# Kernel optimization log

Measured on AMD Instinct MI355X. Metric: run time of the kernel, lower is better.

Reference implementation:

```python
import jax, jax.numpy as jnp
import numpy as np

D_MODEL = 1024
D_FF = 4096
NUM_HEADS = 16
D_HEAD = D_MODEL // NUM_HEADS
EPS = 1e-5


def setup_inputs() -> dict:
    key = jax.random.key(0)
    ks = jax.random.split(key, 16)
    s = 0.02
    return {
        "X": jax.random.normal(ks[0], (2, 2048, D_MODEL), dtype=jnp.float32),
        "W_qkv": jax.random.normal(ks[1], (D_MODEL, 3 * D_MODEL), dtype=jnp.float32) * s,
        "b_qkv": jax.random.normal(ks[2], (3 * D_MODEL,), dtype=jnp.float32) * s,
        "W_o": jax.random.normal(ks[3], (D_MODEL, D_MODEL), dtype=jnp.float32) * s,
        "b_o": jax.random.normal(ks[4], (D_MODEL,), dtype=jnp.float32) * s,
        "W_1": jax.random.normal(ks[5], (D_MODEL, D_FF), dtype=jnp.float32) * s,
        "b_1": jax.random.normal(ks[6], (D_FF,), dtype=jnp.float32) * s,
        "W_2": jax.random.normal(ks[7], (D_FF, D_MODEL), dtype=jnp.float32) * s,
        "b_2": jax.random.normal(ks[8], (D_MODEL,), dtype=jnp.float32) * s,
        "ln1_g": jnp.ones((D_MODEL,), dtype=jnp.float32),
        "ln1_b": jnp.zeros((D_MODEL,), dtype=jnp.float32),
        "ln2_g": jnp.ones((D_MODEL,), dtype=jnp.float32),
        "ln2_b": jnp.zeros((D_MODEL,), dtype=jnp.float32),
    }


def _layernorm(x, g, b):
    mu = jnp.mean(x, axis=-1, keepdims=True)
    var = jnp.mean(jnp.square(x - mu), axis=-1, keepdims=True)
    return (x - mu) * jax.lax.rsqrt(var + EPS) * g + b


def reference(X, W_qkv, b_qkv, W_o, b_o, W_1, b_1, W_2, b_2, ln1_g, ln1_b, ln2_g, ln2_b):
    B, T, D = X.shape
    qkv = X @ W_qkv + b_qkv                      # [B,T,3D]
    Q, K, V = jnp.split(qkv, 3, axis=-1)
    # [B,H,T,d]
    Q = Q.reshape(B, T, NUM_HEADS, D_HEAD).transpose(0, 2, 1, 3)
    K = K.reshape(B, T, NUM_HEADS, D_HEAD).transpose(0, 2, 1, 3)
    V = V.reshape(B, T, NUM_HEADS, D_HEAD).transpose(0, 2, 1, 3)
    scores = jnp.einsum('bhqd,bhkd->bhqk', Q, K) / np.float32(D_HEAD) ** 0.5
    causal = jnp.tril(jnp.ones((T, T), dtype=bool))
    scores = jnp.where(causal, scores, jnp.float32(-jnp.inf))
    A = jax.nn.softmax(scores, axis=-1)
    O = jnp.einsum('bhqk,bhkd->bhqd', A, V)
    O = O.transpose(0, 2, 1, 3).reshape(B, T, D)
    O = O @ W_o + b_o
    H_1 = _layernorm(X + O, ln1_g, ln1_b)
    H_2 = (jax.nn.gelu(H_1 @ W_1 + b_1, approximate=False)) @ W_2 + b_2
    return _layernorm(H_1 + H_2, ln2_g, ln2_b)
```

## Files before the change

### kernel.cpp

```cpp
#include <hip/hip_runtime.h>
#include <cmath>

typedef unsigned short u16;
typedef __bf16 bf16x8 __attribute__((ext_vector_type(8)));
typedef float f32x4 __attribute__((ext_vector_type(4)));

#define DEVI __device__ __forceinline__

DEVI float b2f(u16 u){ union{unsigned int i; float f;} v; v.i=(unsigned int)u<<16; return v.f; }
DEVI u16 f2b(float f){ union{unsigned int i; float f;} v; v.f=f;
    unsigned int r=(v.i+0x7FFFu+((v.i>>16)&1u))>>16; return (u16)r; }

DEVI void gload_lds16(const u16* g, u16* l){
    __builtin_amdgcn_global_load_lds((__attribute__((address_space(1))) void*)g,
                                     (__attribute__((address_space(3))) void*)l,
                                     16, 0, 0);
}

__global__ __launch_bounds__(256)
void cvt_bf16(const float* __restrict__ in, u16* __restrict__ out)
{
    const int i = (blockIdx.x * 256 + threadIdx.x) * 4;
    float4 v = *(const float4*)&in[i];
    ushort4 o;
    o.x = f2b(v.x); o.y = f2b(v.y); o.z = f2b(v.z); o.w = f2b(v.w);
    *(ushort4*)&out[i] = o;
}

__global__ __launch_bounds__(256)
void cvt_transpose(const float* __restrict__ in, u16* __restrict__ out, int R, int C)
{
    __shared__ __align__(16) u16 tile[64*72];
    const int rb = blockIdx.x*64, cb = blockIdx.y*64;
    const int t = threadIdx.x;
    const int r = t >> 3, c0 = (t & 7) * 8;
    #pragma unroll
    for (int rr = 0; rr < 2; rr++) {
        const int row = r + rr*32;
        float4 a = *(const float4*)&in[(long)(rb + row)*C + cb + c0];
        float4 b = *(const float4*)&in[(long)(rb + row)*C + cb + c0 + 4];
        u16* tp = &tile[row*72 + c0];
        tp[0]=f2b(a.x); tp[1]=f2b(a.y); tp[2]=f2b(a.z); tp[3]=f2b(a.w);
        tp[4]=f2b(b.x); tp[5]=f2b(b.y); tp[6]=f2b(b.z); tp[7]=f2b(b.w);
    }
    __syncthreads();
    #pragma unroll
    for (int rr = 0; rr < 2; rr++) {
        const int cr = r + rr*32;
        u16 tmp[8];
        #pragma unroll
        for (int j = 0; j < 8; j++) tmp[j] = tile[(c0 + j)*72 + cr];
        *(uint4*)&out[(long)(cb + cr)*R + rb + c0] = *(uint4*)tmp;
    }
}

template<int EPI, int BM>
__global__ __launch_bounds__(256)
void gemm_bt(const u16* __restrict__ A, const u16* __restrict__ Bt,
             const float* __restrict__ bias, const u16* __restrict__ Res,
             u16* __restrict__ C, int M, int N, int K)
{
    constexpr int RM = BM / 32;
    constexpr int NA = (BM / 16) * 2 / 4;
    __shared__ __align__(16) u16 As[BM*64];
    __shared__ __align__(16) u16 Bs[128*64];
    const int tid  = threadIdx.x;
    const int wave = tid >> 6, lane = tid & 63;
    const int tm = blockIdx.x * BM, tn = blockIdx.y * 128;

    const int rs = lane >> 2, cs = (lane & 3) * 8;
    const u16* gA[NA]; u16* lA[NA];
    #pragma unroll
    for (int i = 0; i < NA; i++) {
        const int c = wave + i*4;
        const int p = c / (BM/16), rb = c % (BM/16);
        gA[i] = A + (long)(tm + rb*16 + rs)*K + p*32 + cs;
        lA[i] = As + p*(BM*32) + rb*512;
    }
    const u16* gB[4]; u16* lB[4];
    #pragma unroll
    for (int i = 0; i < 4; i++) {
        const int c = wave + i*4;
        const int p = c >> 3, rb = c & 7;
        gB[i] = Bt + (long)(tn + rb*16 + rs)*K + p*32 + cs;
        lB[i] = Bs + p*(128*32) + rb*512;
    }

    const int wm = (wave >> 1) * (BM/2), wn = (wave & 1) * 64;
    const int fr = lane & 15, fq = lane >> 4;

    f32x4 acc[RM][4] = {};
    for (int k0 = 0; k0 < K; k0 += 64) {
        __syncthreads();
        #pragma unroll
        for (int i = 0; i < NA; i++) gload_lds16(gA[i] + k0, lA[i]);
        #pragma unroll
        for (int i = 0; i < 4; i++)  gload_lds16(gB[i] + k0, lB[i]);
        __syncthreads();
        #pragma unroll
        for (int p = 0; p < 2; p++) {
            bf16x8 af[RM], bfr[4];
            #pragma unroll
            for (int i = 0; i < RM; i++)
                af[i]  = *(const bf16x8*)&As[p*(BM*32) + (wm + i*16 + fr)*32 + fq*8];
            #pragma unroll
            for (int j = 0; j < 4; j++)
                bfr[j] = *(const bf16x8*)&Bs[p*(128*32) + (wn + j*16 + fr)*32 + fq*8];
            #pragma unroll
            for (int i = 0; i < RM; i++)
                #pragma unroll
                for (int j = 0; j < 4; j++)
                    acc[i][j] = __builtin_amdgcn_mfma_f32_16x16x32_bf16(af[i], bfr[j], acc[i][j], 0, 0, 0);
        }
    }

    #pragma unroll
    for (int i = 0; i < RM; i++) {
        const int row = tm + wm + i*16 + fq*4;
        #pragma unroll
        for (int j = 0; j < 4; j++) {
            const int col = tn + wn + j*16 + fr;
            const float bv = bias[col];
            #pragma unroll
            for (int r = 0; r < 4; r++) {
                float v = acc[i][j][r] + bv;
                const long idx = (long)(row + r)*N + col;
                if (EPI == 1) v += b2f(Res[idx]);
                if (EPI == 2) {
                    const float u = v + 0.044715f*v*v*v;
                    const float t = exp2f(u * 2.302208f);
                    v = v * t * __builtin_amdgcn_rcpf(t + 1.f);
                }
                C[idx] = f2b(v);
            }
        }
    }
}

__global__ __launch_bounds__(256)
void attn_kernel(const u16* __restrict__ qkv, u16* __restrict__ O)
{
    constexpr float LOG2E = 1.4426950408889634f;
    __shared__ __align__(16) u16 Qs[64*72];
    __shared__ __align__(16) u16 Ks[64*72];
    __shared__ __align__(16) u16 Vs[64*72];
    __shared__ __align__(16) u16 Ps[4][16*72];

    const int tid = threadIdx.x, wave = tid >> 6, lane = tid & 63;
    const int qt = blockIdx.x, h = blockIdx.y, b = blockIdx.z;
    const long base = (long)b*2048*3072 + h*64;
    const int fr = lane & 15, fq = lane >> 4;

    {
        const int r = tid >> 3, c = (tid & 7) * 8;
        #pragma unroll
        for (int rr = 0; rr < 2; rr++) {
            uint4 v = *(const uint4*)&qkv[base + (long)(qt*64 + r + rr*32)*3072 + c];
            u16 tmp[8]; *(uint4*)tmp = v;
            u16* qp = &Qs[(r + rr*32)*72 + c];
            #pragma unroll
            for (int j = 0; j < 8; j++) qp[j] = f2b(b2f(tmp[j]) * 0.125f);
        }
    }
    __syncthreads();

    bf16x8 bq[2];
    #pragma unroll
    for (int ks = 0; ks < 2; ks++)
        bq[ks] = *(const bf16x8*)&Qs[(wave*16 + fr)*72 + ks*32 + fq*8];

    const int q_glob = qt*64 + wave*16 + fr;
    f32x4 o[4] = {};
    float m_i = -1e30f, l_i = 0.f;

    for (int kt = 0; kt <= qt; kt++) {
        __syncthreads();
        {
            const int r = tid >> 3, c = (tid & 7) * 8;
            #pragma unroll
            for (int rr = 0; rr < 2; rr++) {
                const int row = r + rr*32;
                uint4 kv = *(const uint4*)&qkv[base + 1024 + (long)(kt*64 + row)*3072 + c];
                *(uint4*)&Ks[row*72 + c] = kv;
                uint4 vv = *(const uint4*)&qkv[base + 2048 + (long)(kt*64 + row)*3072 + c];
                u16 tmp[8]; *(uint4*)tmp = vv;
                #pragma unroll
                for (int j = 0; j < 8; j++) {
                    const int d = c + j;
                    Vs[d*72 + (row ^ (d & 56))] = tmp[j];
                }
            }
        }
        __syncthreads();

        f32x4 st[4] = {};
        #pragma unroll
        for (int nt = 0; nt < 4; nt++)
            #pragma unroll
            for (int ks = 0; ks < 2; ks++) {
                bf16x8 ak = *(const bf16x8*)&Ks[(nt*16 + fr)*72 + ks*32 + fq*8];
                st[nt] = __builtin_amdgcn_mfma_f32_16x16x32_bf16(ak, bq[ks], st[nt], 0, 0, 0);
            }

        float sv[4][4];
        float mx = -1e30f;
        #pragma unroll
        for (int nt = 0; nt < 4; nt++) {
            #pragma unroll
            for (int r = 0; r < 4; r++) {
                const int key = kt*64 + nt*16 + fq*4 + r;
                float v = st[nt][r];
                if (key > q_glob) v = -1e30f;
                sv[nt][r] = v;
                mx = fmaxf(mx, v);
            }
        }
        mx = fmaxf(mx, __shfl_xor(mx, 16, 64));
        mx = fmaxf(mx, __shfl_xor(mx, 32, 64));
        const float mnew  = fmaxf(m_i, mx);
        const float alpha = exp2f((m_i - mnew) * LOG2E);
        float ps = 0.f;
        #pragma unroll
        for (int nt = 0; nt < 4; nt++)
            #pragma unroll
            for (int r = 0; r < 4; r++) {
                const float p = exp2f((sv[nt][r] - mnew) * LOG2E);
                sv[nt][r] = p; ps += p;
            }
        ps += __shfl_xor(ps, 16, 64);
        ps += __shfl_xor(ps, 32, 64);
        l_i = l_i * alpha + ps;
        m_i = mnew;

        #pragma unroll
        for (int r = 0; r < 4; r++) {
            const float ar = __shfl(alpha, (lane & 48) + fq*4 + r, 64);
            #pragma unroll
            for (int dt = 0; dt < 4; dt++) o[dt][r] *= ar;
        }

        u16* pw = Ps[wave];
        #pragma unroll
        for (int nt = 0; nt < 4; nt++)
            #pragma unroll
            for (int d = 0; d < 2; d++) {
                const unsigned pk = (unsigned)f2b(sv[nt][2*d]) |
                                    ((unsigned)f2b(sv[nt][2*d+1]) << 16);
                *(unsigned*)&pw[fr*72 + nt*16 + fq*4 + 2*d] = pk;
            }
        __asm__ volatile("" ::: "memory");

        bf16x8 ap[2];
        #pragma unroll
        for (int kk = 0; kk < 2; kk++)
            ap[kk] = *(const bf16x8*)&pw[fr*72 + kk*32 + fq*8];

        #pragma unroll
        for (int dt = 0; dt < 4; dt++) {
            const int d = dt*16 + fr;
            #pragma unroll
            for (int kk = 0; kk < 2; kk++) {
                const int kb = (kk*32 + fq*8) ^ (d & 56);
                bf16x8 bv = *(const bf16x8*)&Vs[d*72 + kb];
                o[dt] = __builtin_amdgcn_mfma_f32_16x16x32_bf16(ap[kk], bv, o[dt], 0, 0, 0);
            }
        }
    }

    float lro[4];
    #pragma unroll
    for (int r = 0; r < 4; r++)
        lro[r] = __shfl(l_i, (lane & 48) + fq*4 + r, 64);
    const long orow0 = (long)b*2048 + qt*64 + wave*16 + fq*4;
    #pragma unroll
    for (int dt = 0; dt < 4; dt++) {
        const int col = h*64 + dt*16 + fr;
        #pragma unroll
        for (int r = 0; r < 4; r++)
            O[(orow0 + r)*1024 + col] = f2b(o[dt][r] / lro[r]);
    }
}

template<int OUTF32>
__global__ __launch_bounds__(256)
void ln_kernel(const u16* __restrict__ X, const float* __restrict__ G,
               const float* __restrict__ B, void* __restrict__ Yv)
{
    __shared__ float red[8];
    const int tid = threadIdx.x;
    const long row = blockIdx.x;
    const u16* x = X + row*1024;
    ushort4 u = *(const ushort4*)&x[tid*4];
    const float v0 = b2f(u.x), v1 = b2f(u.y), v2 = b2f(u.z), v3 = b2f(u.w);
    float s = v0+v1+v2+v3;
    float q = v0*v0+v1*v1+v2*v2+v3*v3;
    #pragma unroll
    for (int off = 32; off >= 1; off >>= 1) {
        s += __shfl_xor(s, off, 64);
        q += __shfl_xor(q, off, 64);
    }
    const int wv = tid >> 6;
    if ((tid & 63) == 0) { red[wv*2] = s; red[wv*2+1] = q; }
    __syncthreads();
    s = red[0]+red[2]+red[4]+red[6];
    q = red[1]+red[3]+red[5]+red[7];
    const float mu = s * (1.f/1024.f);
    const float rstd = rsqrtf(fmaxf(q*(1.f/1024.f) - mu*mu, 0.f) + 1e-5f);
    float4 g4 = *(const float4*)&G[tid*4];
    float4 b4 = *(const float4*)&B[tid*4];
    const float y0 = (v0-mu)*rstd*g4.x + b4.x;
    const float y1 = (v1-mu)*rstd*g4.y + b4.y;
    const float y2 = (v2-mu)*rstd*g4.z + b4.z;
    const float y3 = (v3-mu)*rstd*g4.w + b4.w;
    if (OUTF32) {
        float4 o = make_float4(y0, y1, y2, y3);
        *(float4*)&((float*)Yv)[row*1024 + tid*4] = o;
    } else {
        ushort4 o;
        o.x = f2b(y0); o.y = f2b(y1); o.z = f2b(y2); o.w = f2b(y3);
        *(ushort4*)&((u16*)Yv)[row*1024 + tid*4] = o;
    }
}

extern "C" void kernel_launch(void* const* d_in, const int* in_sizes, int n_in,
                              void* d_out, int out_size, void* d_ws, size_t ws_size,
                              hipStream_t stream)
{
    const float* X    = (const float*)d_in[0];
    const float* Wqkv = (const float*)d_in[1];
    const float* bqkv = (const float*)d_in[2];
    const float* Wo   = (const float*)d_in[3];
    const float* bo   = (const float*)d_in[4];
    const float* W1   = (const float*)d_in[5];
    const float* b1   = (const float*)d_in[6];
    const float* W2   = (const float*)d_in[7];
    const float* b2   = (const float*)d_in[8];
    const float* g1   = (const float*)d_in[9];
    const float* be1  = (const float*)d_in[10];
    const float* g2   = (const float*)d_in[11];
    const float* be2  = (const float*)d_in[12];
    float* out = (float*)d_out;

    char* ws = (char*)d_ws;
    u16* Xbf   = (u16*)(ws + 0);
    u16* WqkvT = (u16*)(ws + 8388608);
    u16* WoT   = (u16*)(ws + 14680064);
    u16* QKV   = (u16*)(ws + 16777216);
    u16* AO    = (u16*)(ws + 41943040);
    u16* S1    = (u16*)(ws + 16777216);
    u16* H1    = (u16*)(ws + 0);
    u16* Gbuf  = (u16*)(ws + 8388608);
    u16* S2    = (u16*)(ws + 41943040);
    u16* W1T   = (u16*)d_out;
    u16* W2T   = (u16*)d_out + 4194304;

    cvt_bf16<<<4096, 256, 0, stream>>>(X, Xbf);
    cvt_transpose<<<dim3(16, 48), 256, 0, stream>>>(Wqkv, WqkvT, 1024, 3072);
    cvt_transpose<<<dim3(16, 16), 256, 0, stream>>>(Wo,   WoT,   1024, 1024);
    cvt_transpose<<<dim3(16, 64), 256, 0, stream>>>(W1,   W1T,   1024, 4096);
    cvt_transpose<<<dim3(64, 16), 256, 0, stream>>>(W2,   W2T,   4096, 1024);

    gemm_bt<0,128><<<dim3(32, 24), 256, 0, stream>>>(Xbf, WqkvT, bqkv, nullptr, QKV, 4096, 3072, 1024);
    attn_kernel<<<dim3(32, 16, 2), 256, 0, stream>>>(QKV, AO);
    gemm_bt<1,64><<<dim3(64, 8), 256, 0, stream>>>(AO, WoT, bo, Xbf, S1, 4096, 1024, 1024);
    ln_kernel<0><<<4096, 256, 0, stream>>>(S1, g1, be1, H1);
    gemm_bt<2,128><<<dim3(32, 32), 256, 0, stream>>>(H1, W1T, b1, nullptr, Gbuf, 4096, 4096, 1024);
    gemm_bt<1,64><<<dim3(64, 8), 256, 0, stream>>>(Gbuf, W2T, b2, H1, S2, 4096, 1024, 4096);
    ln_kernel<1><<<4096, 256, 0, stream>>>(S2, g2, be2, out);
}
```

Measured before the change: 415.1 us.

## Use 128-key tiles in attention, transpose PV MFMA, skip masking on full tiles

```diff
diff --git a/kernel.cpp b/kernel.cpp
--- a/kernel.cpp
+++ b/kernel.cpp
@@ -142,9 +142,8 @@
 {
     constexpr float LOG2E = 1.4426950408889634f;
     __shared__ __align__(16) u16 Qs[64*72];
-    __shared__ __align__(16) u16 Ks[64*72];
-    __shared__ __align__(16) u16 Vs[64*72];
-    __shared__ __align__(16) u16 Ps[4][16*72];
+    __shared__ __align__(16) u16 Ks[128*72];
+    __shared__ __align__(16) u16 Vs[64*136];
 
     const int tid = threadIdx.x, wave = tid >> 6, lane = tid & 63;
     const int qt = blockIdx.x, h = blockIdx.y, b = blockIdx.z;
@@ -170,50 +169,60 @@
         bq[ks] = *(const bf16x8*)&Qs[(wave*16 + fr)*72 + ks*32 + fq*8];
 
     const int q_glob = qt*64 + wave*16 + fr;
+    const int q_wmin = qt*64 + wave*16;
     f32x4 o[4] = {};
     float m_i = -1e30f, l_i = 0.f;
-
-    for (int kt = 0; kt <= qt; kt++) {
+    const int nkt = (qt >> 1) + 1;
+
+    for (int kt = 0; kt < nkt; kt++) {
+        const int k0 = kt * 128;
         __syncthreads();
         {
             const int r = tid >> 3, c = (tid & 7) * 8;
             #pragma unroll
-            for (int rr = 0; rr < 2; rr++) {
+            for (int rr = 0; rr < 4; rr++) {
                 const int row = r + rr*32;
-                uint4 kv = *(const uint4*)&qkv[base + 1024 + (long)(kt*64 + row)*3072 + c];
+                uint4 kv = *(const uint4*)&qkv[base + 1024 + (long)(k0 + row)*3072 + c];
                 *(uint4*)&Ks[row*72 + c] = kv;
-                uint4 vv = *(const uint4*)&qkv[base + 2048 + (long)(kt*64 + row)*3072 + c];
+                uint4 vv = *(const uint4*)&qkv[base + 2048 + (long)(k0 + row)*3072 + c];
                 u16 tmp[8]; *(uint4*)tmp = vv;
                 #pragma unroll
                 for (int j = 0; j < 8; j++) {
                     const int d = c + j;
-                    Vs[d*72 + (row ^ (d & 56))] = tmp[j];
+                    Vs[d*136 + (row ^ (d & 56))] = tmp[j];
                 }
             }
         }
         __syncthreads();
 
-        f32x4 st[4] = {};
-        #pragma unroll
-        for (int nt = 0; nt < 4; nt++)
+        f32x4 st[8];
+        #pragma unroll
+        for (int mt = 0; mt < 8; mt++) st[mt] = (f32x4){0.f,0.f,0.f,0.f};
+        #pragma unroll
+        for (int mt = 0; mt < 8; mt++)
             #pragma unroll
             for (int ks = 0; ks < 2; ks++) {
-                bf16x8 ak = *(const bf16x8*)&Ks[(nt*16 + fr)*72 + ks*32 + fq*8];
-                st[nt] = __builtin_amdgcn_mfma_f32_16x16x32_bf16(ak, bq[ks], st[nt], 0, 0, 0);
-            }
-
-        float sv[4][4];
+                bf16x8 ak = *(const bf16x8*)&Ks[(mt*16 + fr)*72 + ks*32 + fq*8];
+                st[mt] = __builtin_amdgcn_mfma_f32_16x16x32_bf16(ak, bq[ks], st[mt], 0, 0, 0);
+            }
+
         float mx = -1e30f;
-        #pragma unroll
-        for (int nt = 0; nt < 4; nt++) {
-            #pragma unroll
-            for (int r = 0; r < 4; r++) {
-                const int key = kt*64 + nt*16 + fq*4 + r;
-                float v = st[nt][r];
-                if (key > q_glob) v = -1e30f;
-                sv[nt][r] = v;
-                mx = fmaxf(mx, v);
-            }
+        if (k0 + 127 > q_wmin) {
+            #pragma unroll
+            for (int mt = 0; mt < 8; mt++)
+                #pragma unroll
+                for (int r = 0; r < 4; r++) {
+                    const int key = k0 + mt*16 + fq*4 + r;
+                    float v = st[mt][r];
+                    if (key > q_glob) v = -1e30f;
+                    st[mt][r] = v;
+                    mx = fmaxf(mx, v);
+                }
+        } else {
+            #pragma unroll
+            for (int mt = 0; mt < 8; mt++)
+                #pragma unroll
+                for (int r = 0; r < 4; r++) mx = fmaxf(mx, st[mt][r]);
         }
         mx = fmaxf(mx, __shfl_xor(mx, 16, 64));
         mx = fmaxf(mx, __shfl_xor(mx, 32, 64));
@@ -221,11 +230,11 @@
         const float alpha = exp2f((m_i - mnew) * LOG2E);
         float ps = 0.f;
         #pragma unroll
-        for (int nt = 0; nt < 4; nt++)
+        for (int mt = 0; mt < 8; mt++)
             #pragma unroll
             for (int r = 0; r < 4; r++) {
-                const float p = exp2f((sv[nt][r] - mnew) * LOG2E);
-                sv[nt][r] = p; ps += p;
+                const float p = exp2f((st[mt][r] - mnew) * LOG2E);
+                st[mt][r] = p; ps += p;
             }
         ps += __shfl_xor(ps, 16, 64);
         ps += __shfl_xor(ps, 32, 64);
@@ -233,51 +242,49 @@
         m_i = mnew;
 
         #pragma unroll
-        for (int r = 0; r < 4; r++) {
-            const float ar = __shfl(alpha, (lane & 48) + fq*4 + r, 64);
-            #pragma unroll
-            for (int dt = 0; dt < 4; dt++) o[dt][r] *= ar;
-        }
-
-        u16* pw = Ps[wave];
-        #pragma unroll
-        for (int nt = 0; nt < 4; nt++)
-            #pragma unroll
-            for (int d = 0; d < 2; d++) {
-                const unsigned pk = (unsigned)f2b(sv[nt][2*d]) |
-                                    ((unsigned)f2b(sv[nt][2*d+1]) << 16);
-                *(unsigned*)&pw[fr*72 + nt*16 + fq*4 + 2*d] = pk;
-            }
-        __asm__ volatile("" ::: "memory");
-
-        bf16x8 ap[2];
-        #pragma unroll
-        for (int kk = 0; kk < 2; kk++)
-            ap[kk] = *(const bf16x8*)&pw[fr*72 + kk*32 + fq*8];
-
-        #pragma unroll
-        for (int dt = 0; dt < 4; dt++) {
-            const int d = dt*16 + fr;
-            #pragma unroll
-            for (int kk = 0; kk < 2; kk++) {
-                const int kb = (kk*32 + fq*8) ^ (d & 56);
-                bf16x8 bv = *(const bf16x8*)&Vs[d*72 + kb];
-                o[dt] = __builtin_amdgcn_mfma_f32_16x16x32_bf16(ap[kk], bv, o[dt], 0, 0, 0);
-            }
-        }
-    }
-
-    float lro[4];
-    #pragma unroll
-    for (int r = 0; r < 4; r++)
-        lro[r] = __shfl(l_i, (lane & 48) + fq*4 + r, 64);
-    const long orow0 = (long)b*2048 + qt*64 + wave*16 + fq*4;
+        for (int dt = 0; dt < 4; dt++)
+            #pragma unroll
+            for (int r = 0; r < 4; r++) o[dt][r] *= alpha;
+
+        u16* pw = &Qs[wave * 1152];
+        #pragma unroll
+        for (int half = 0; half < 2; half++) {
+            #pragma unroll
+            for (int mt2 = 0; mt2 < 4; mt2++)
+                #pragma unroll
+                for (int d = 0; d < 2; d++) {
+                    const int mt = half*4 + mt2;
+                    const unsigned pk = (unsigned)f2b(st[mt][2*d]) |
+                                        ((unsigned)f2b(st[mt][2*d+1]) << 16);
+                    *(unsigned*)&pw[fr*72 + mt2*16 + fq*4 + 2*d] = pk;
+                }
+            __asm__ volatile("" ::: "memory");
+            bf16x8 bp[2];
+            #pragma unroll
+            for (int kk = 0; kk < 2; kk++)
+                bp[kk] = *(const bf16x8*)&pw[fr*72 + kk*32 + fq*8];
+            #pragma unroll
+            for (int dt = 0; dt < 4; dt++) {
+                const int d = dt*16 + fr;
+                #pragma unroll
+                for (int kk = 0; kk < 2; kk++) {
+                    const int kb = (half*64 + kk*32 + fq*8) ^ (d & 56);
+                    bf16x8 av = *(const bf16x8*)&Vs[d*136 + kb];
+                    o[dt] = __builtin_amdgcn_mfma_f32_16x16x32_bf16(av, bp[kk], o[dt], 0, 0, 0);
+                }
+            }
+            __asm__ volatile("" ::: "memory");
+        }
+    }
+
+    const float rl = __builtin_amdgcn_rcpf(l_i);
+    const long orow = (long)b*2048 + qt*64 + wave*16 + fr;
     #pragma unroll
     for (int dt = 0; dt < 4; dt++) {
-        const int col = h*64 + dt*16 + fr;
-        #pragma unroll
-        for (int r = 0; r < 4; r++)
-            O[(orow0 + r)*1024 + col] = f2b(o[dt][r] / lro[r]);
+        u16 pk[4];
+        #pragma unroll
+        for (int r = 0; r < 4; r++) pk[r] = f2b(o[dt][r] * rl);
+        *(uint2*)&O[orow*1024 + h*64 + dt*16 + fq*4] = *(uint2*)pk;
     }
 }
 
```

After: 420.2 us. Within noise of the previous version (+1.2%).
